# Performance work log

Measured on AMD Instinct MI355X. Metric: run time of the kernel, lower is better.

The kernel has to match this reference:

```python
import jax, jax.numpy as jnp
import numpy as np

EPS = 1e-8

def _ste(x, q):
    # straight-through estimator: forward = q, backward = identity
    return x + jax.lax.stop_gradient(q - x)

def quant_act_uint8(x):
    # per-tensor uint8 activation fake-quant (Brevitas Uint8ActPerTensorFloat style)
    s = jax.lax.stop_gradient(jnp.maximum(jnp.max(x), EPS)) / 255.0
    q = jnp.clip(jnp.round(x / s), 0.0, 255.0) * s
    return _ste(x, q), s

def quant_weight_int8_perchannel(w):
    # per-output-channel symmetric int8 fake-quant; w: [out, in]
    s = jax.lax.stop_gradient(jnp.maximum(jnp.max(jnp.abs(w), axis=1, keepdims=True), EPS)) / 127.0
    q = jnp.clip(jnp.round(w / s), -128.0, 127.0) * s
    return _ste(w, q), s[:, 0]

def quant_bias_int32(b, s_in, s_w):
    # bias quantized at scale s_in * s_w[c] (Brevitas Int32Bias)
    s = jax.lax.stop_gradient(s_in * s_w)
    q = jnp.round(b / s) * s
    return _ste(b, q)

def quant_linear(x, w, b):
    xq, s_in = quant_act_uint8(x)
    wq, s_w = quant_weight_int8_perchannel(w)
    bq = quant_bias_int32(b, s_in, s_w)
    return jnp.einsum('btd,fd->btf', xq, wq) + bq

def setup_inputs() -> dict:
    key = jax.random.key(0)
    k1, k2, k3, k4, k5 = jax.random.split(key, 5)
    B, S, D, F = 4, 2048, 1024, 4096
    return {
        'x': jax.random.normal(k1, (B, S, D), dtype=jnp.float32),
        'w1': jax.random.normal(k2, (F, D), dtype=jnp.float32) * (1.0 / np.sqrt(D)),
        'b1': jax.random.normal(k3, (F,), dtype=jnp.float32) * 0.01,
        'w2': jax.random.normal(k4, (D, F), dtype=jnp.float32) * (1.0 / np.sqrt(F)),
        'b2': jax.random.normal(k5, (D,), dtype=jnp.float32) * 0.01,
    }

def reference(x, w1, b1, w2, b2):
    h = jax.nn.relu(quant_linear(x, w1, b1))
    # dropout is identity in eval mode
    return quant_linear(h, w2, b2)
```

## Files before the change

kernel.cpp:

```cpp
#include <hip/hip_runtime.h>
#include <stdint.h>

#define EPSQ 1e-8f

typedef __attribute__((ext_vector_type(4))) int i32x4;

__device__ __forceinline__ unsigned enc_f(float f) {
    unsigned u = __float_as_uint(f);
    return (u & 0x80000000u) ? ~u : (u | 0x80000000u);
}
__device__ __forceinline__ float dec_f(unsigned u) {
    return (u & 0x80000000u) ? __uint_as_float(u & 0x7fffffffu)
                             : __uint_as_float(~u);
}

__device__ __forceinline__ float wave_max_f(float v) {
    #pragma unroll
    for (int off = 32; off; off >>= 1) v = fmaxf(v, __shfl_xor(v, off));
    return v;
}
__device__ __forceinline__ int wave_sum_i(int v) {
    #pragma unroll
    for (int off = 32; off; off >>= 1) v += __shfl_xor(v, off);
    return v;
}

__global__ __launch_bounds__(256) void k_prep(
    const float4* __restrict__ x, long n4x, float* __restrict__ partials,
    const float* __restrict__ w1, signed char* __restrict__ w1q,
    float* __restrict__ sw1, int* __restrict__ rs1,
    const float* __restrict__ w2, signed char* __restrict__ w2q,
    float* __restrict__ sw2, int* __restrict__ rs2) {
    __shared__ float sm[4];
    __shared__ int   si[4];
    int b = blockIdx.x;
    int wid = threadIdx.x >> 6;
    if (b < 2048) {
        long i = (long)b * 256 + threadIdx.x;
        float m = -3.4e38f;
        for (; i < n4x; i += 2048L * 256) {
            float4 v = x[i];
            m = fmaxf(fmaxf(m, fmaxf(v.x, v.y)), fmaxf(v.z, v.w));
        }
        m = wave_max_f(m);
        if ((threadIdx.x & 63) == 0) sm[wid] = m;
        __syncthreads();
        if (threadIdx.x == 0)
            partials[b] = fmaxf(fmaxf(sm[0], sm[1]), fmaxf(sm[2], sm[3]));
        return;
    }
    const float* w; signed char* q; float* s_out; int* rs_out; int row, L;
    if (b < 2048 + 4096) { row = b - 2048; w = w1; q = w1q; s_out = sw1; rs_out = rs1; L = 1024; }
    else                 { row = b - 6144; w = w2; q = w2q; s_out = sw2; rs_out = rs2; L = 4096; }

    const float4* wr = (const float4*)(w + (long)row * L);
    int n4 = L >> 2;
    float m = 0.0f;
    for (int i = threadIdx.x; i < n4; i += 256) {
        float4 v = wr[i];
        m = fmaxf(m, fmaxf(fmaxf(fabsf(v.x), fabsf(v.y)),
                           fmaxf(fabsf(v.z), fabsf(v.w))));
    }
    m = wave_max_f(m);
    if ((threadIdx.x & 63) == 0) sm[wid] = m;
    __syncthreads();
    m = fmaxf(fmaxf(sm[0], sm[1]), fmaxf(sm[2], sm[3]));
    float s = fmaxf(m, EPSQ) / 127.0f;

    char4* qr = (char4*)(q + (long)row * L);
    int isum = 0;
    for (int i = threadIdx.x; i < n4; i += 256) {
        float4 v = wr[i];
        int a = min(max((int)rintf(v.x / s), -128), 127);
        int bb = min(max((int)rintf(v.y / s), -128), 127);
        int c = min(max((int)rintf(v.z / s), -128), 127);
        int d = min(max((int)rintf(v.w / s), -128), 127);
        isum += a + bb + c + d;
        char4 cc; cc.x = (char)a; cc.y = (char)bb; cc.z = (char)c; cc.w = (char)d;
        qr[i] = cc;
    }
    isum = wave_sum_i(isum);
    if ((threadIdx.x & 63) == 0) si[wid] = isum;
    __syncthreads();
    if (threadIdx.x == 0) {
        s_out[row]  = s;
        rs_out[row] = si[0] + si[1] + si[2] + si[3];
    }
}

__global__ __launch_bounds__(256) void k_quant_act(
    const float4* __restrict__ in, char4* __restrict__ out, long n4,
    const float* __restrict__ partials, unsigned* __restrict__ slots) {
    __shared__ float sm[4];
    float m = -3.4e38f;
    for (int i = threadIdx.x; i < 2048; i += 256) m = fmaxf(m, partials[i]);
    m = wave_max_f(m);
    if ((threadIdx.x & 63) == 0) sm[threadIdx.x >> 6] = m;
    __syncthreads();
    m = fmaxf(fmaxf(sm[0], sm[1]), fmaxf(sm[2], sm[3]));
    if (blockIdx.x == 0 && threadIdx.x == 0) {
        slots[0] = enc_f(m);
        slots[1] = 0u;
    }
    float s = fmaxf(m, EPSQ) / 255.0f;
    long i = (long)blockIdx.x * 256 + threadIdx.x;
    for (; i < n4; i += (long)gridDim.x * 256) {
        float4 v = in[i];
        int a = min(max((int)rintf(v.x / s), 0), 255) - 128;
        int b = min(max((int)rintf(v.y / s), 0), 255) - 128;
        int c = min(max((int)rintf(v.z / s), 0), 255) - 128;
        int d = min(max((int)rintf(v.w / s), 0), 255) - 128;
        char4 cc; cc.x = (char)a; cc.y = (char)b; cc.z = (char)c; cc.w = (char)d;
        out[i] = cc;
    }
}

__device__ __forceinline__ void gl_lds16(const signed char* g, signed char* l) {
    __builtin_amdgcn_global_load_lds(
        (const __attribute__((address_space(1))) unsigned int*)g,
        (__attribute__((address_space(3))) unsigned int*)l, 16, 0, 0);
}

template<int MODE, int BM, int NW>
__global__ __launch_bounds__(NW * 64, (MODE == 0 ? 3 : 4)) void k_gemm_i8(
    const signed char* __restrict__ A,
    const signed char* __restrict__ B,
    const float* __restrict__ s_w,
    const int* __restrict__ rowsum,
    const float* __restrict__ bias,
    const unsigned* __restrict__ act_slot,
    float* __restrict__ Cf,
    signed char* __restrict__ Cq,
    unsigned* __restrict__ omax_slot,
    int M, int N, long K) {
    __shared__ __align__(16) signed char Als[BM * 128];
    __shared__ __align__(16) signed char Bls[128 * 128];
    __shared__ float red[NW];

    const int t    = threadIdx.x;
    const int lane = t & 63;
    const int w    = t >> 6;
    const int m0   = blockIdx.y * BM;
    const int n0   = blockIdx.x * 128;
    const int mr   = lane & 15;
    const int qq   = lane >> 4;
    constexpr int PB = 8 / NW;

    const signed char* a0 = A + (long)(m0 + w * 32 + mr) * K + qq * 16;
    const signed char* b0 = B + (long)(n0 + w * PB * 16 + mr) * K + qq * 16;
    signed char* ad = Als + w * 4096 + lane * 16;
    signed char* bd = Bls + w * PB * 2048 + lane * 16;

    const int wrow = (w >> 1) * 64;
    const int wcol = (w & 1) * 64;
    const int a_base = (w >> 1) * 8192 + lane * 16;
    const int b_base = (w & 1) * 8192 + lane * 16;

    i32x4 acc[4][4];
    #pragma unroll
    for (int i = 0; i < 4; i++)
        #pragma unroll
        for (int j = 0; j < 4; j++) acc[i][j] = (i32x4){0, 0, 0, 0};

    for (long k0 = 0; k0 < K; k0 += 128) {
        __syncthreads();
        gl_lds16(a0 + k0,               ad);
        gl_lds16(a0 + k0 + 64,          ad + 1024);
        gl_lds16(a0 + k0 + 16 * K,      ad + 2048);
        gl_lds16(a0 + k0 + 16 * K + 64, ad + 3072);
        #pragma unroll
        for (int p = 0; p < PB; p++) {
            gl_lds16(b0 + k0 + (long)p * 16 * K,      bd + p * 2048);
            gl_lds16(b0 + k0 + (long)p * 16 * K + 64, bd + p * 2048 + 1024);
        }
        __syncthreads();

        #pragma unroll
        for (int kk = 0; kk < 2; kk++) {
            i32x4 af[4], bf[4];
            #pragma unroll
            for (int i = 0; i < 4; i++)
                af[i] = *(const i32x4*)(Als + a_base + i * 2048 + kk * 1024);
            #pragma unroll
            for (int j = 0; j < 4; j++)
                bf[j] = *(const i32x4*)(Bls + b_base + j * 2048 + kk * 1024);
            #pragma unroll
            for (int i = 0; i < 4; i++)
                #pragma unroll
                for (int j = 0; j < 4; j++)
                    acc[i][j] = __builtin_amdgcn_mfma_i32_16x16x64_i8(
                        af[i], bf[j], acc[i][j], 0, 0, 0);
        }
    }

    const float s_act = fmaxf(dec_f(*act_slot), EPSQ) / 255.0f;

    if (MODE == 1) {
        float lmax = 0.0f;
        #pragma unroll
        for (int j = 0; j < 4; j++) {
            int im = -2147483647 - 1;
            #pragma unroll
            for (int i = 0; i < 4; i++)
                #pragma unroll
                for (int r = 0; r < 4; r++) im = max(im, acc[i][j][r]);
            int gn = n0 + wcol + j * 16 + mr;
            float ssc  = s_act * s_w[gn];
            float bint = rintf(bias[gn] / ssc);
            float h = ssc * ((float)(im + 128 * rowsum[gn]) + bint);
            lmax = fmaxf(lmax, h);
        }
        lmax = fmaxf(lmax, 0.0f);
        lmax = wave_max_f(lmax);
        if (lane == 0) red[w] = lmax;
        __syncthreads();
        if (t == 0) {
            float bm = red[0];
            #pragma unroll
            for (int i = 1; i < NW; i++) bm = fmaxf(bm, red[i]);
            atomicMax(omax_slot, enc_f(bm));
        }
        return;
    }

    float s_oq = 1.0f;
    if (MODE == 2) s_oq = fmaxf(dec_f(*omax_slot), EPSQ) / 255.0f;

    #pragma unroll
    for (int j = 0; j < 4; j++) {
        int gn = n0 + wcol + j * 16 + mr;
        float ssc  = s_act * s_w[gn];
        float bint = rintf(bias[gn] / ssc);
        int   icor = 128 * rowsum[gn];
        float fq   = (MODE == 2) ? (ssc / s_oq) : 0.0f;
        #pragma unroll
        for (int i = 0; i < 4; i++) {
            #pragma unroll
            for (int r = 0; r < 4; r++) {
                int gm = m0 + wrow + i * 16 + qq * 4 + r;
                float v = (float)(acc[i][j][r] + icor) + bint;
                if (MODE == 0) {
                    Cf[(long)gm * N + gn] = ssc * v;
                } else {
                    int qv = min(max((int)rintf(fq * v), 0), 255) - 128;
                    Cq[(long)gm * N + gn] = (signed char)qv;
                }
            }
        }
    }
}

extern "C" void kernel_launch(void* const* d_in, const int* in_sizes, int n_in,
                              void* d_out, int out_size, void* d_ws, size_t ws_size,
                              hipStream_t stream) {
    const float* x  = (const float*)d_in[0];
    const float* w1 = (const float*)d_in[1];
    const float* b1 = (const float*)d_in[2];
    const float* w2 = (const float*)d_in[3];
    const float* b2 = (const float*)d_in[4];
    float* out = (float*)d_out;

    const int M = 8192, D = 1024, F = 4096;

    char* ws = (char*)d_ws;
    size_t off = 0;
    unsigned* slots = (unsigned*)ws;               off += 256;
    float* partials = (float*)(ws + off);          off += 2048 * 4;
    signed char* xi  = (signed char*)(ws + off);   off += (size_t)M * D;
    signed char* w1q = (signed char*)(ws + off);   off += (size_t)F * D;
    signed char* w2q = (signed char*)(ws + off);   off += (size_t)D * F;
    float* sw1 = (float*)(ws + off);               off += (size_t)F * 4;
    float* sw2 = (float*)(ws + off);               off += (size_t)D * 4;
    int* rs1   = (int*)(ws + off);                 off += (size_t)F * 4;
    int* rs2   = (int*)(ws + off);                 off += (size_t)D * 4;
    signed char* hq = (signed char*)(ws + off);    off += (size_t)M * F;

    k_prep<<<dim3(2048 + F + D), dim3(256), 0, stream>>>(
        (const float4*)x, (long)M * D / 4, partials,
        w1, w1q, sw1, rs1, w2, w2q, sw2, rs2);
    k_quant_act<<<dim3(2048), dim3(256), 0, stream>>>(
        (const float4*)x, (char4*)xi, (long)M * D / 4, partials, slots);
    k_gemm_i8<1, 256, 8><<<dim3(F / 128, M / 256), dim3(512), 0, stream>>>(
        xi, w1q, sw1, rs1, b1, slots + 0, nullptr, nullptr, slots + 1, M, F, (long)D);
    k_gemm_i8<2, 256, 8><<<dim3(F / 128, M / 256), dim3(512), 0, stream>>>(
        xi, w1q, sw1, rs1, b1, slots + 0, nullptr, hq, slots + 1, M, F, (long)D);
    k_gemm_i8<0, 128, 4><<<dim3(D / 128, M / 128), dim3(256), 0, stream>>>(
        hq, w2q, sw2, rs2, b2, slots + 1, out, nullptr, nullptr, M, D, (long)F);

    (void)in_sizes; (void)n_in; (void)out_size; (void)ws_size;
}
```

Before: 295.5 us.

## Compute first GEMM once, stash 16-bit scaled activations, then requantize

Previously the first int8 GEMM ran twice: once to find the global post-ReLU max and once to quantize its output with that max. Now a single pass writes ReLU outputs as 16-bit values normalized by a per-block max and records each block's max. A separate elementwise kernel then rescales those values to uint8 using the global max. This removes one full GEMM of compute but adds a 16-bit intermediate write and read, and the extra rounding step can make some requantized values differ by one from the exact result.

```diff
diff --git a/kernel.cpp b/kernel.cpp
--- a/kernel.cpp
+++ b/kernel.cpp
@@ -115,6 +115,27 @@
     }
 }
 
+__global__ __launch_bounds__(256) void k_requant(
+    const ushort4* __restrict__ h16, char4* __restrict__ hq,
+    const float* __restrict__ sblk, const unsigned* __restrict__ slots, long n4) {
+    float s_h = fmaxf(dec_f(slots[1]), EPSQ) / 255.0f;
+    float inv = 1.0f / (65535.0f * s_h);
+    long i = (long)blockIdx.x * 256 + threadIdx.x;
+    for (; i < n4; i += (long)gridDim.x * 256) {
+        long e = i << 2;
+        int m = (int)(e >> 12);
+        int f = (int)(e & 4095);
+        float fq = sblk[(m >> 8) * 32 + (f >> 7)] * inv;
+        ushort4 u = h16[i];
+        char4 cc;
+        cc.x = (char)(min(max((int)rintf(u.x * fq), 0), 255) - 128);
+        cc.y = (char)(min(max((int)rintf(u.y * fq), 0), 255) - 128);
+        cc.z = (char)(min(max((int)rintf(u.z * fq), 0), 255) - 128);
+        cc.w = (char)(min(max((int)rintf(u.w * fq), 0), 255) - 128);
+        hq[i] = cc;
+    }
+}
+
 __device__ __forceinline__ void gl_lds16(const signed char* g, signed char* l) {
     __builtin_amdgcn_global_load_lds(
         (const __attribute__((address_space(1))) unsigned int*)g,
@@ -130,7 +151,8 @@
     const float* __restrict__ bias,
     const unsigned* __restrict__ act_slot,
     float* __restrict__ Cf,
-    signed char* __restrict__ Cq,
+    unsigned short* __restrict__ H16,
+    float* __restrict__ sblk,
     unsigned* __restrict__ omax_slot,
     int M, int N, long K) {
     __shared__ __align__(16) signed char Als[BM * 128];
@@ -195,36 +217,53 @@
 
     const float s_act = fmaxf(dec_f(*act_slot), EPSQ) / 255.0f;
 
-    if (MODE == 1) {
+    if (MODE == 3) {
+        float sscv[4], bintv[4]; int icorv[4];
         float lmax = 0.0f;
         #pragma unroll
         for (int j = 0; j < 4; j++) {
+            int gn = n0 + wcol + j * 16 + mr;
+            float ssc  = s_act * s_w[gn];
+            float bint = rintf(bias[gn] / ssc);
+            int   icor = 128 * rowsum[gn];
+            sscv[j] = ssc; bintv[j] = bint; icorv[j] = icor;
             int im = -2147483647 - 1;
             #pragma unroll
             for (int i = 0; i < 4; i++)
                 #pragma unroll
                 for (int r = 0; r < 4; r++) im = max(im, acc[i][j][r]);
-            int gn = n0 + wcol + j * 16 + mr;
-            float ssc  = s_act * s_w[gn];
-            float bint = rintf(bias[gn] / ssc);
-            float h = ssc * ((float)(im + 128 * rowsum[gn]) + bint);
-            lmax = fmaxf(lmax, h);
+            lmax = fmaxf(lmax, ssc * ((float)(im + icor) + bint));
         }
         lmax = fmaxf(lmax, 0.0f);
         lmax = wave_max_f(lmax);
         if (lane == 0) red[w] = lmax;
         __syncthreads();
+        float bm = red[0];
+        #pragma unroll
+        for (int i = 1; i < NW; i++) bm = fmaxf(bm, red[i]);
         if (t == 0) {
-            float bm = red[0];
-            #pragma unroll
-            for (int i = 1; i < NW; i++) bm = fmaxf(bm, red[i]);
+            sblk[blockIdx.y * gridDim.x + blockIdx.x] = bm;
             atomicMax(omax_slot, enc_f(bm));
         }
+        float inv = 65535.0f / fmaxf(bm, EPSQ);
+        #pragma unroll
+        for (int j = 0; j < 4; j++) {
+            int gn = n0 + wcol + j * 16 + mr;
+            #pragma unroll
+            for (int i = 0; i < 4; i++) {
+                #pragma unroll
+                for (int r = 0; r < 4; r++) {
+                    int gm = m0 + wrow + i * 16 + qq * 4 + r;
+                    float h = fmaxf(
+                        sscv[j] * ((float)(acc[i][j][r] + icorv[j]) + bintv[j]),
+                        0.0f);
+                    int u = min((int)rintf(h * inv), 65535);
+                    H16[(long)gm * N + gn] = (unsigned short)u;
+                }
+            }
+        }
         return;
     }
-
-    float s_oq = 1.0f;
-    if (MODE == 2) s_oq = fmaxf(dec_f(*omax_slot), EPSQ) / 255.0f;
 
     #pragma unroll
     for (int j = 0; j < 4; j++) {
@@ -232,19 +271,13 @@
         float ssc  = s_act * s_w[gn];
         float bint = rintf(bias[gn] / ssc);
         int   icor = 128 * rowsum[gn];
-        float fq   = (MODE == 2) ? (ssc / s_oq) : 0.0f;
         #pragma unroll
         for (int i = 0; i < 4; i++) {
             #pragma unroll
             for (int r = 0; r < 4; r++) {
                 int gm = m0 + wrow + i * 16 + qq * 4 + r;
-                float v = (float)(acc[i][j][r] + icor) + bint;
-                if (MODE == 0) {
-                    Cf[(long)gm * N + gn] = ssc * v;
-                } else {
-                    int qv = min(max((int)rintf(fq * v), 0), 255) - 128;
-                    Cq[(long)gm * N + gn] = (signed char)qv;
-                }
+                Cf[(long)gm * N + gn] =
+                    ssc * ((float)(acc[i][j][r] + icor) + bint);
             }
         }
     }
@@ -274,18 +307,22 @@
     int* rs1   = (int*)(ws + off);                 off += (size_t)F * 4;
     int* rs2   = (int*)(ws + off);                 off += (size_t)D * 4;
     signed char* hq = (signed char*)(ws + off);    off += (size_t)M * F;
+    unsigned short* h16 = (unsigned short*)(ws + off); off += (size_t)M * F * 2;
+    float* sblk = (float*)(ws + off);              off += 1024 * 4;
 
     k_prep<<<dim3(2048 + F + D), dim3(256), 0, stream>>>(
         (const float4*)x, (long)M * D / 4, partials,
         w1, w1q, sw1, rs1, w2, w2q, sw2, rs2);
     k_quant_act<<<dim3(2048), dim3(256), 0, stream>>>(
         (const float4*)x, (char4*)xi, (long)M * D / 4, partials, slots);
-    k_gemm_i8<1, 256, 8><<<dim3(F / 128, M / 256), dim3(512), 0, stream>>>(
-        xi, w1q, sw1, rs1, b1, slots + 0, nullptr, nullptr, slots + 1, M, F, (long)D);
-    k_gemm_i8<2, 256, 8><<<dim3(F / 128, M / 256), dim3(512), 0, stream>>>(
-        xi, w1q, sw1, rs1, b1, slots + 0, nullptr, hq, slots + 1, M, F, (long)D);
+    k_gemm_i8<3, 256, 8><<<dim3(F / 128, M / 256), dim3(512), 0, stream>>>(
+        xi, w1q, sw1, rs1, b1, slots + 0, nullptr, h16, sblk, slots + 1,
+        M, F, (long)D);
+    k_requant<<<dim3(2048), dim3(256), 0, stream>>>(
+        (const ushort4*)h16, (char4*)hq, sblk, slots, (long)M * F / 4);
     k_gemm_i8<0, 128, 4><<<dim3(D / 128, M / 128), dim3(256), 0, stream>>>(
-        hq, w2q, sw2, rs2, b2, slots + 1, out, nullptr, nullptr, M, D, (long)F);
+        hq, w2q, sw2, rs2, b2, slots + 1, out, nullptr, nullptr, nullptr,
+        M, D, (long)F);
 
     (void)in_sizes; (void)n_in; (void)out_size; (void)ws_size;
 }
```

After: 274.9 us. 1.07x faster.
